# Kernel tuning notes

Hardware: AMD Instinct MI355X
Metric: run time of the kernel (lower is better)

The kernel has to match this reference:

```python
import jax, jax.numpy as jnp
import numpy as np

M, NQ, NK = 2, 1024, 1024
DX, DT = 256, 2
H, D = 8, 32          # num_heads, head_dim
KH = 32               # kernel MLP hidden width
SCALE = D ** -0.5


def setup_inputs() -> dict:
    key = jax.random.key(0)
    ks = jax.random.split(key, 16)
    p = 0.02
    return {
        "xq": jax.random.normal(ks[0], (M, NQ, DX), jnp.float32),
        "xk": jax.random.normal(ks[1], (M, NK, DX), jnp.float32),
        "xv": jax.random.normal(ks[2], (M, NK, DX), jnp.float32),
        "tq": jax.random.normal(ks[3], (M, NQ, DT), jnp.float32),
        "tk": jax.random.normal(ks[4], (M, NK, DT), jnp.float32),
        # projections (no bias, as in nn.Linear(..., bias=False))
        "Wq": jax.random.normal(ks[5], (DX, H * D), jnp.float32) * p,
        "Wk": jax.random.normal(ks[6], (DX, H * D), jnp.float32) * p,
        "Wv": jax.random.normal(ks[7], (DX, H * D), jnp.float32) * p,
        # output projection (with bias)
        "Wo": jax.random.normal(ks[8], (H * D, DX), jnp.float32) * p,
        "bo": jnp.zeros((DX,), jnp.float32),
        # kernel MLP: dt -> KH -> H
        "Wk1": jax.random.normal(ks[9], (DT, KH), jnp.float32) * 0.5,
        "bk1": jnp.zeros((KH,), jnp.float32),
        "Wk2": jax.random.normal(ks[10], (KH, H), jnp.float32) * 0.5,
        "bk2": jnp.zeros((H,), jnp.float32),
        # phi_t: H -> DT
        "Wphi": jax.random.normal(ks[11], (H, DT), jnp.float32) * p,
        "bphi": jnp.zeros((DT,), jnp.float32),
    }


def reference(xq, xk, xv, tq, tk, Wq, Wk, Wv, Wo, bo, Wk1, bk1, Wk2, bk2, Wphi, bphi):
    m, nq, _ = xq.shape
    nk = xk.shape[1]
    # translation group action: diff [m, nq, nk, dt]
    diff = tq[:, :, None, :] - tk[:, None, :, :]
    # q, k: [m, h, n, d]
    q = (xq @ Wq).reshape(m, nq, H, D).transpose(0, 2, 1, 3)
    k = (xk @ Wk).reshape(m, nk, H, D).transpose(0, 2, 1, 3)
    token_dots = jnp.einsum("bhqd,bhkd->bhqk", q, k) * SCALE
    # kernel MLP bias evaluated densely over diffs -> [m, nq, nk, h] -> [m, h, nq, nk]
    hdn = jax.nn.relu(diff @ Wk1 + bk1)
    kdots = (hdn @ Wk2 + bk2).transpose(0, 3, 1, 2)
    dots = kdots + token_dots
    attn = jax.nn.softmax(dots, axis=-1)  # [m, h, nq, nk]
    v = (xv @ Wv).reshape(m, nk, H, D).transpose(0, 2, 1, 3)
    out = jnp.einsum("bhqk,bhkd->bhqd", attn, v)
    out = out.transpose(0, 2, 1, 3).reshape(m, nq, H * D)
    out = out @ Wo + bo  # dropout p=0
    # phi_t path: attn -> [m, nq, nk, h] -> per-pair dt weights
    attn_t = attn.transpose(0, 2, 3, 1)
    t_dots = attn_t @ Wphi + bphi  # [m, nq, nk, dt]
    tq_new = tq + (1.0 / nk) * jnp.sum(diff * t_dots, axis=-2)
    return out, tq_new
```

## Files before the change

kernel.cpp:

```cpp
#include <hip/hip_runtime.h>
#include <hip/hip_bf16.h>

#define MB 2
#define NQ 1024
#define NK 1024
#define DXC 256
#define HD 256
#define HH 8
#define DD 32
#define KHC 32
#define LOG2E 1.4426950408889634f
#define QSCALE 0.25503472301046627f

#define QB 32
#define KB 32
#define KSPLIT 8
#define KL 128
#define NCHUNK 4

#define QPB_F   0u
#define KPB_F   262144u
#define VPT_F   524288u
#define WT_F    786432u
#define AQH_F   917504u
#define BKH_F   950272u
#define TS_F    983040u
#define TKX_F   983048u
#define W2T_F   986120u
#define PART_F  986376u

typedef float f32x4 __attribute__((ext_vector_type(4)));
typedef short bf16x8 __attribute__((ext_vector_type(8)));
typedef _Float16 f16x8 __attribute__((ext_vector_type(8)));
typedef _Float16 f16x2 __attribute__((ext_vector_type(2)));

#define MFMA(a, b, c)   __builtin_amdgcn_mfma_f32_16x16x32_bf16(a, b, c, 0, 0, 0)
#define MFMA16(a, b, c) __builtin_amdgcn_mfma_f32_16x16x32_f16(a, b, c, 0, 0, 0)
#define EXP2(x) exp2f(x)

#define KDQ 36
#define KDH 1160

struct Ptrs {
    const float *xq, *xk, *xv, *tq, *tk;
    const float *Wq, *Wk, *Wv, *Wo, *bo;
    const float *Wk1, *bk1, *Wk2, *bk2, *Wphi, *bphi;
    float* wsf;
    float* out;
};

__device__ __forceinline__ uint cvt_pk_bf16(float lo, float hi) {
    uint r;
    asm("v_cvt_pk_bf16_f32 %0, %1, %2" : "=v"(r) : "v"(lo), "v"(hi));
    return r;
}
__device__ __forceinline__ ushort f2bf1(float f) { return (ushort)cvt_pk_bf16(f, 0.f); }
__device__ __forceinline__ float bf2f(uint x) {
    return __uint_as_float((x & 0xffffu) << 16);
}
__device__ __forceinline__ ushort f2h(float f) {
    _Float16 h = (_Float16)f;
    return __builtin_bit_cast(ushort, h);
}

__global__ __launch_bounds__(256, 4) void k_phase1(Ptrs p) {
    __shared__ __align__(16) float sW[64][65];
    const int u = blockIdx.x;
    const int t = threadIdx.x;
    ushort* wt  = (ushort*)(p.wsf + WT_F);
    ushort* aqh = (ushort*)(p.wsf + AQH_F);
    ushort* bkh = (ushort*)(p.wsf + BKH_F);
    ushort* tkx = (ushort*)(p.wsf + TKX_F);
    ushort* w2t = (ushort*)(p.wsf + W2T_F);
    float*  ts  = p.wsf + TS_F;

    if (u < 64) {
        const int mat = u >> 4;
        const float* W = (mat == 0) ? p.Wq : (mat == 1) ? p.Wk : (mat == 2) ? p.Wv : p.Wo;
        const int k0 = (u & 3) * 64, c0 = ((u >> 2) & 3) * 64;
        #pragma unroll
        for (int i = 0; i < 4; ++i) {
            int flat = i * 1024 + t * 4;
            int r = flat >> 6, c = flat & 63;
            float4 v4 = *(const float4*)(W + (size_t)(k0 + r) * 256 + c0 + c);
            sW[r][c] = v4.x; sW[r][c + 1] = v4.y; sW[r][c + 2] = v4.z; sW[r][c + 3] = v4.w;
        }
        __syncthreads();
        #pragma unroll
        for (int i = 0; i < 4; ++i) {
            int flat = i * 1024 + t * 4;
            int cc = flat >> 6, kk = flat & 63;
            uint2 pk;
            pk.x = cvt_pk_bf16(sW[kk][cc], sW[kk + 1][cc]);
            pk.y = cvt_pk_bf16(sW[kk + 2][cc], sW[kk + 3][cc]);
            *(uint2*)(wt + (size_t)mat * 65536 + (size_t)(c0 + cc) * 256 + k0 + kk) = pk;
        }
    } else if (u < 320) {
        int gid = (u - 64) * 256 + t;
        int row = gid >> 5, j = gid & 31;
        aqh[gid] = f2h(p.tq[row * 2] * p.Wk1[j] + p.tq[row * 2 + 1] * p.Wk1[KHC + j] + p.bk1[j]);
        bkh[gid] = f2h(p.tk[row * 2] * p.Wk1[j] + p.tk[row * 2 + 1] * p.Wk1[KHC + j]);
    } else if (u < 344) {
        int g = (u - 320) * 256 + t;
        int mm = g / 3072, rr = (g % 3072) >> 10, kk = g & 1023;
        float v = (rr == 0) ? p.tk[(size_t)(mm * NK + kk) * 2]
                : (rr == 1) ? p.tk[(size_t)(mm * NK + kk) * 2 + 1] : 1.0f;
        tkx[g] = f2bf1(v);
    } else if (u == 344) {
        for (int g = t; g < 512; g += 256) {
            int hh2 = g >> 5, jj = g & 31;
            w2t[g] = f2h(hh2 < HH ? p.Wk2[jj * HH + hh2] * LOG2E : 0.f);
        }
    } else {
        const int m = u - 345;
        const int c = t & 1, kk = t >> 1;
        float s = 0.f;
        #pragma unroll
        for (int i = 0; i < 8; ++i) s += p.tk[(size_t)(m * NK + kk + i * 128) * 2 + c];
        float* red = (float*)&sW[0][0];
        red[t] = s; __syncthreads();
        for (int off = 128; off >= 2; off >>= 1) {
            if (t < off) red[t] += red[t + off];
            __syncthreads();
        }
        if (t < 2) ts[m * 2 + t] = red[t];
    }
}

__global__ __launch_bounds__(256, 4) void k_phase2(Ptrs p) {
    __shared__ __align__(16) ushort sTr[256][24];
    const int u = blockIdx.x;
    const int t = threadIdx.x;
    ushort* qpb = (ushort*)(p.wsf + QPB_F);
    ushort* kpb = (ushort*)(p.wsf + KPB_F);
    ushort* vpt = (ushort*)(p.wsf + VPT_F);
    const ushort* wt = (const ushort*)(p.wsf + WT_F);

    const int z = u / 128;
    const int R0 = (u % 128) * 16;
    const float* x = (z == 0) ? p.xq : (z == 1) ? p.xk : p.xv;
    const ushort* wz = wt + (size_t)z * 65536;
    const int wid = t >> 6, l = t & 63, g = l >> 4, c16 = l & 15;
    const int wc = wid * 64;
    const int row = R0 + c16;

    f32x4 acc[4];
    #pragma unroll
    for (int i = 0; i < 4; ++i) acc[i] = (f32x4){0.f, 0.f, 0.f, 0.f};

    for (int k0 = 0; k0 < DXC; k0 += 32) {
        const float* xr = x + (size_t)row * DXC + k0 + g * 8;
        float4 a0 = *(const float4*)xr;
        float4 a1 = *(const float4*)(xr + 4);
        union { bf16x8 v; uint d[4]; } af;
        af.d[0] = cvt_pk_bf16(a0.x, a0.y);
        af.d[1] = cvt_pk_bf16(a0.z, a0.w);
        af.d[2] = cvt_pk_bf16(a1.x, a1.y);
        af.d[3] = cvt_pk_bf16(a1.z, a1.w);
        #pragma unroll
        for (int cf = 0; cf < 4; ++cf) {
            bf16x8 bf = *(const bf16x8*)(wz + (size_t)(wc + cf * 16 + c16) * 256 + k0 + g * 8);
            acc[cf] = MFMA(af.v, bf, acc[cf]);
        }
    }
    if (z != 2) {
        #pragma unroll
        for (int cf = 0; cf < 4; ++cf) {
            #pragma unroll
            for (int r = 0; r < 4; ++r) {
                int orow = R0 + g * 4 + r;
                int col = wc + cf * 16 + c16;
                float v = acc[cf][r];
                if (z == 0) qpb[(size_t)orow * HD + col] = f2bf1(v * QSCALE);
                else        kpb[(size_t)orow * HD + col] = f2bf1(v);
            }
        }
    } else {
        #pragma unroll
        for (int cf = 0; cf < 4; ++cf)
            #pragma unroll
            for (int r = 0; r < 4; ++r)
                sTr[wc + cf * 16 + c16][g * 4 + r] = f2bf1(acc[cf][r]);
        __syncthreads();
        const int mq = R0 >> 10, rin = R0 & 1023;
        ushort* dst = vpt + (size_t)mq * (HD * NK) + (size_t)t * NK + rin;
        *(uint4*)dst       = *(const uint4*)&sTr[t][0];
        *(uint4*)(dst + 8) = *(const uint4*)&sTr[t][8];
    }
}

__global__ __launch_bounds__(256, 2) void k_phase3(Ptrs p) {
    __shared__ __align__(16) char smem[47360];
    const int u = blockIdx.x;
    const int t = threadIdx.x;

    const ushort* qpb = (const ushort*)(p.wsf + QPB_F);
    const ushort* kpb = (const ushort*)(p.wsf + KPB_F);
    const ushort* vpt = (const ushort*)(p.wsf + VPT_F);
    const ushort* aqh = (const ushort*)(p.wsf + AQH_F);
    const ushort* bkh = (const ushort*)(p.wsf + BKH_F);
    const ushort* tkx = (const ushort*)(p.wsf + TKX_F);
    const ushort* w2t = (const ushort*)(p.wsf + W2T_F);
    ushort* part = (ushort*)(p.wsf + PART_F);

    const int ks = u & 7;
    const int qt = (u >> 3) & 31;
    const int m  = u >> 8;
    const int q0 = qt * QB;
    const int kbase = ks * KL;
    const int wid = t >> 6;
    const int l = t & 63;
    const int g = l >> 4;
    const int c16 = l & 15;

    ushort* KD0 = (ushort*)smem;
    ushort* KD1 = (ushort*)(smem + 18560);
    ushort (*sP)[32][40] = (ushort(*)[32][40])(smem + 37120);

    f16x8 w2v = *(const f16x8*)(w2t + c16 * 32 + g * 8);
    const float b2l = (c16 < HH) ? p.bk2[c16] * LOG2E : 0.f;
    const f16x8 zero8 = {0, 0, 0, 0, 0, 0, 0, 0};

    bf16x8 qb[2][2];
    #pragma unroll
    for (int hh = 0; hh < 2; ++hh)
        #pragma unroll
        for (int qf = 0; qf < 2; ++qf)
            qb[hh][qf] = *(const bf16x8*)(qpb + (size_t)(m * NQ + q0 + qf * 16 + c16) * HD
                                              + (wid * 2 + hh) * DD + g * 8);
    f16x8 aqv[8];
    #pragma unroll
    for (int qi = 0; qi < 8; ++qi)
        aqv[qi] = *(const f16x8*)(aqh + (size_t)(m * NQ + q0 + wid * 8 + qi) * KHC + g * 8);

    struct BkOps { f16x8 b0, b1; };
    struct KavOps { bf16x8 ka0[2], ka1[2], v0[2], v1[2], vt; };
    const size_t vbase = (size_t)m * (HD * NK);
    const size_t tbase = (size_t)m * 3072 + (size_t)(c16 < 2 ? c16 : 2) * NK;

    auto loadBk = [&](int k0) {
        BkOps c;
        c.b0 = *(const f16x8*)(bkh + (size_t)(m * NK + k0 + c16) * KHC + g * 8);
        c.b1 = *(const f16x8*)(bkh + (size_t)(m * NK + k0 + 16 + c16) * KHC + g * 8);
        return c;
    };
    auto loadKav = [&](int k0) {
        KavOps c;
        #pragma unroll
        for (int hh = 0; hh < 2; ++hh) {
            const int h = wid * 2 + hh;
            c.ka0[hh] = *(const bf16x8*)(kpb + (size_t)(m * NK + k0 + c16) * HD + h * DD + g * 8);
            c.ka1[hh] = *(const bf16x8*)(kpb + (size_t)(m * NK + k0 + 16 + c16) * HD + h * DD + g * 8);
            c.v0[hh]  = *(const bf16x8*)(vpt + vbase + (size_t)(h * DD + c16) * NK + k0 + g * 8);
            c.v1[hh]  = *(const bf16x8*)(vpt + vbase + (size_t)(h * DD + 16 + c16) * NK + k0 + g * 8);
        }
        c.vt = *(const bf16x8*)(tkx + tbase + k0 + g * 8);
        return c;
    };

    f32x4 oacc[2][2][3];
    #pragma unroll
    for (int a = 0; a < 2; ++a)
        #pragma unroll
        for (int bb = 0; bb < 2; ++bb)
            #pragma unroll
            for (int c = 0; c < 3; ++c)
                oacc[a][bb][c] = (f32x4){0.f, 0.f, 0.f, 0.f};

    auto kdPhase = [&](const BkOps& bk, ushort* kdb) {
        __builtin_amdgcn_s_setprio(1);
        #pragma unroll
        for (int qi = 0; qi < 8; ++qi) {
            const int q = wid * 8 + qi;
            #pragma unroll
            for (int kh = 0; kh < 2; ++kh) {
                f16x8 d = aqv[qi] - (kh ? bk.b1 : bk.b0);
                f16x8 hv = __builtin_elementwise_max(d, zero8);
                f32x4 c = {b2l, b2l, b2l, b2l};
                c = MFMA16(hv, w2v, c);
                if (c16 < HH) {
                    uint2 st;
                    st.x = __builtin_bit_cast(uint, __builtin_amdgcn_cvt_pkrtz(c[0], c[1]));
                    st.y = __builtin_bit_cast(uint, __builtin_amdgcn_cvt_pkrtz(c[2], c[3]));
                    *(uint2*)&kdb[c16 * KDH + q * KDQ + kh * 16 + g * 4] = st;
                }
            }
        }
        __builtin_amdgcn_s_setprio(0);
    };
    auto qkpv = [&](const KavOps& kv, const ushort* kdbuf) {
        __builtin_amdgcn_s_setprio(1);
        #pragma unroll
        for (int hh = 0; hh < 2; ++hh) {
            const int h = wid * 2 + hh;
            const ushort* kdb = &kdbuf[h * KDH];
            #pragma unroll
            for (int kf = 0; kf < 2; ++kf) {
                #pragma unroll
                for (int qf = 0; qf < 2; ++qf) {
                    uint2 kd2 = *(const uint2*)&kdb[(qf * 16 + c16) * KDQ + kf * 16 + g * 4];
                    f16x2 k01 = __builtin_bit_cast(f16x2, kd2.x);
                    f16x2 k23 = __builtin_bit_cast(f16x2, kd2.y);
                    f32x4 cinit = {(float)k01[0], (float)k01[1], (float)k23[0], (float)k23[1]};
                    f32x4 s = MFMA((kf ? kv.ka1[hh] : kv.ka0[hh]), qb[hh][qf], cinit);
                    uint2 pk;
                    pk.x = cvt_pk_bf16(EXP2(s[0]), EXP2(s[1]));
                    pk.y = cvt_pk_bf16(EXP2(s[2]), EXP2(s[3]));
                    *(uint2*)&sP[wid][qf * 16 + c16][kf * 16 + g * 4] = pk;
                }
            }
            #pragma unroll
            for (int qf = 0; qf < 2; ++qf) {
                bf16x8 pa = *(const bf16x8*)&sP[wid][qf * 16 + c16][g * 8];
                oacc[hh][qf][0] = MFMA(pa, kv.v0[hh], oacc[hh][qf][0]);
                oacc[hh][qf][1] = MFMA(pa, kv.v1[hh], oacc[hh][qf][1]);
                oacc[hh][qf][2] = MFMA(pa, kv.vt, oacc[hh][qf][2]);
            }
        }
        __builtin_amdgcn_s_setprio(0);
    };

    BkOps bk0v = loadBk(kbase);
    KavOps kv0 = loadKav(kbase);
    BkOps bk1v = loadBk(kbase + KB);
    KavOps kv1 = loadKav(kbase + KB);
    kdPhase(bk0v, KD0);
    __syncthreads();

    kdPhase(bk1v, KD1);
    BkOps bk2v = loadBk(kbase + 2 * KB);
    qkpv(kv0, KD0);
    kv0 = loadKav(kbase + 2 * KB);
    __syncthreads();
    kdPhase(bk2v, KD0);
    BkOps bk3v = loadBk(kbase + 3 * KB);
    qkpv(kv1, KD1);
    kv1 = loadKav(kbase + 3 * KB);
    __syncthreads();
    kdPhase(bk3v, KD1);
    qkpv(kv0, KD0);
    __syncthreads();
    qkpv(kv1, KD1);

    #pragma unroll
    for (int hh = 0; hh < 2; ++hh) {
        int mh = m * HH + wid * 2 + hh;
        #pragma unroll
        for (int qf = 0; qf < 2; ++qf) {
            #pragma unroll
            for (int r = 0; r < 4; ++r) {
                int q = q0 + qf * 16 + g * 4 + r;
                ushort* pb = part + ((size_t)(mh * KSPLIT + ks) * NQ + q) * 40;
                pb[c16]      = f2bf1(oacc[hh][qf][0][r]);
                pb[16 + c16] = f2bf1(oacc[hh][qf][1][r]);
                float e = oacc[hh][qf][2][r];
                if (c16 < 2) pb[32 + c16] = f2bf1(e);
                else if (c16 == 2) *(float*)(pb + 34) = e;
            }
        }
    }
}

__global__ __launch_bounds__(256, 4) void k_phase4(Ptrs p) {
    __shared__ __align__(16) ushort sHob[16][264];
    __shared__ float sD[8][8][2];
    const int u = blockIdx.x;
    const int t = threadIdx.x;
    const ushort* part = (const ushort*)(p.wsf + PART_F);
    const ushort* wt = (const ushort*)(p.wsf + WT_F);
    const float* ts = p.wsf + TS_F;
    float* tq_out = p.out + (size_t)MB * NQ * HD;

    const int m = u >> 7;
    const int q0 = (u & 127) * 8;

    if (t < 128) {
        const int h = t >> 4, dgrp = (t >> 3) & 1, qloc = t & 7;
        const int q = q0 + qloc;
        const int mh = m * HH + h;
        float accO[16] = {};
        float aT = 0.f, lsum = 0.f;
        for (int s = 0; s < KSPLIT; ++s) {
            const ushort* ps = part + ((size_t)(mh * KSPLIT + s) * NQ + q) * 40;
            uint4 v0 = *(const uint4*)(ps + dgrp * 16);
            uint4 v1 = *(const uint4*)(ps + dgrp * 16 + 8);
            accO[0] += bf2f(v0.x); accO[1] += bf2f(v0.x >> 16);
            accO[2] += bf2f(v0.y); accO[3] += bf2f(v0.y >> 16);
            accO[4] += bf2f(v0.z); accO[5] += bf2f(v0.z >> 16);
            accO[6] += bf2f(v0.w); accO[7] += bf2f(v0.w >> 16);
            accO[8] += bf2f(v1.x); accO[9] += bf2f(v1.x >> 16);
            accO[10] += bf2f(v1.y); accO[11] += bf2f(v1.y >> 16);
            accO[12] += bf2f(v1.z); accO[13] += bf2f(v1.z >> 16);
            accO[14] += bf2f(v1.w); accO[15] += bf2f(v1.w >> 16);
            uint at = *(const uint*)(ps + 32);
            aT += bf2f(dgrp == 0 ? at : (at >> 16));
            lsum += *(const float*)(ps + 34);
        }
        const float inv = 1.f / lsum;
        uint dd[8];
        #pragma unroll
        for (int i = 0; i < 8; ++i)
            dd[i] = cvt_pk_bf16(accO[2 * i] * inv, accO[2 * i + 1] * inv);
        ushort* hp = &sHob[qloc][h * DD + dgrp * 16];
        *(uint4*)hp       = (uint4){dd[0], dd[1], dd[2], dd[3]};
        *(uint4*)(hp + 8) = (uint4){dd[4], dd[5], dd[6], dd[7]};
        const float A = aT * inv;
        const float tqc = p.tq[(size_t)(m * NQ + q) * 2 + dgrp];
        sD[h][qloc][dgrp] = p.Wphi[h * 2 + dgrp] * (tqc - A);
    } else {
        for (int i = t - 128; i < 8 * 264; i += 128)
            (&sHob[8][0])[i] = 0;
    }
    __syncthreads();

    if (t < 16) {
        int ql2 = t >> 1, c = t & 1;
        float s = 0.f;
        #pragma unroll
        for (int hh2 = 0; hh2 < 8; ++hh2) s += sD[hh2][ql2][c];
        int qg = q0 + ql2;
        float tqv = p.tq[(size_t)(m * NQ + qg) * 2 + c];
        const float invnk = 1.f / (float)NK;
        tq_out[(size_t)(m * NQ + qg) * 2 + c] =
            tqv + s * invnk + p.bphi[c] * (tqv - ts[m * 2 + c] * invnk);
    }

    const ushort* wz3 = wt + (size_t)3 * 65536;
    const int wid = t >> 6, l = t & 63, g = l >> 4, c16 = l & 15;
    f32x4 acc[4];
    #pragma unroll
    for (int i = 0; i < 4; ++i) acc[i] = (f32x4){0.f, 0.f, 0.f, 0.f};
    for (int k0 = 0; k0 < HD; k0 += 32) {
        bf16x8 af = *(const bf16x8*)&sHob[c16][k0 + g * 8];
        #pragma unroll
        for (int cf = 0; cf < 4; ++cf) {
            int col = wid * 64 + cf * 16 + c16;
            bf16x8 bf = *(const bf16x8*)(wz3 + (size_t)col * 256 + k0 + g * 8);
            acc[cf] = MFMA(af, bf, acc[cf]);
        }
    }
    if (g < 2) {
        #pragma unroll
        for (int cf = 0; cf < 4; ++cf) {
            int col = wid * 64 + cf * 16 + c16;
            float bv = p.bo[col];
            #pragma unroll
            for (int r = 0; r < 4; ++r) {
                int orow = q0 + g * 4 + r;
                p.out[(size_t)(m * NQ + orow) * DXC + col] = acc[cf][r] + bv;
            }
        }
    }
}

extern "C" void kernel_launch(void* const* d_in, const int* in_sizes, int n_in,
                              void* d_out, int out_size, void* d_ws, size_t ws_size,
                              hipStream_t stream)
{
    Ptrs p;
    p.xq   = (const float*)d_in[0];
    p.xk   = (const float*)d_in[1];
    p.xv   = (const float*)d_in[2];
    p.tq   = (const float*)d_in[3];
    p.tk   = (const float*)d_in[4];
    p.Wq   = (const float*)d_in[5];
    p.Wk   = (const float*)d_in[6];
    p.Wv   = (const float*)d_in[7];
    p.Wo   = (const float*)d_in[8];
    p.bo   = (const float*)d_in[9];
    p.Wk1  = (const float*)d_in[10];
    p.bk1  = (const float*)d_in[11];
    p.Wk2  = (const float*)d_in[12];
    p.bk2  = (const float*)d_in[13];
    p.Wphi = (const float*)d_in[14];
    p.bphi = (const float*)d_in[15];
    p.wsf  = (float*)d_ws;
    p.out  = (float*)d_out;

    hipLaunchKernelGGL(k_phase1, dim3(347), dim3(256), 0, stream, p);
    hipLaunchKernelGGL(k_phase2, dim3(384), dim3(256), 0, stream, p);
    hipLaunchKernelGGL(k_phase3, dim3(512), dim3(256), 0, stream, p);
    hipLaunchKernelGGL(k_phase4, dim3(256), dim3(256), 0, stream, p);
}
```

Before: 56.55 us.

## Split phase3 attention across eight waves with one head per wave

The attention phase kernel grows from 256 to 512 threads per block. Each wave now handles one head instead of two, and the kernel-MLP bias computation is split over 8 waves with 4 queries each. This halves per-thread register state (q fragments, K/V operands, accumulators) and doubles the waves available to hide memory and MFMA latency. In exchange, shared memory per block grows for the extra per-wave P tiles, and the tighter launch bound may cap registers or limit resident blocks.

```diff
diff --git a/kernel.cpp b/kernel.cpp
--- a/kernel.cpp
+++ b/kernel.cpp
@@ -189,8 +189,8 @@
     }
 }
 
-__global__ __launch_bounds__(256, 2) void k_phase3(Ptrs p) {
-    __shared__ __align__(16) char smem[47360];
+__global__ __launch_bounds__(512, 4) void k_phase3(Ptrs p) {
+    __shared__ __align__(16) char smem[57600];
     const int u = blockIdx.x;
     const int t = threadIdx.x;
 
@@ -212,6 +212,7 @@
     const int l = t & 63;
     const int g = l >> 4;
     const int c16 = l & 15;
+    const int h = wid;
 
     ushort* KD0 = (ushort*)smem;
     ushort* KD1 = (ushort*)(smem + 18560);
@@ -221,20 +222,18 @@
     const float b2l = (c16 < HH) ? p.bk2[c16] * LOG2E : 0.f;
     const f16x8 zero8 = {0, 0, 0, 0, 0, 0, 0, 0};
 
-    bf16x8 qb[2][2];
+    bf16x8 qb[2];
     #pragma unroll
-    for (int hh = 0; hh < 2; ++hh)
-        #pragma unroll
-        for (int qf = 0; qf < 2; ++qf)
-            qb[hh][qf] = *(const bf16x8*)(qpb + (size_t)(m * NQ + q0 + qf * 16 + c16) * HD
-                                              + (wid * 2 + hh) * DD + g * 8);
-    f16x8 aqv[8];
+    for (int qf = 0; qf < 2; ++qf)
+        qb[qf] = *(const bf16x8*)(qpb + (size_t)(m * NQ + q0 + qf * 16 + c16) * HD
+                                      + h * DD + g * 8);
+    f16x8 aqv[4];
     #pragma unroll
-    for (int qi = 0; qi < 8; ++qi)
-        aqv[qi] = *(const f16x8*)(aqh + (size_t)(m * NQ + q0 + wid * 8 + qi) * KHC + g * 8);
+    for (int qi = 0; qi < 4; ++qi)
+        aqv[qi] = *(const f16x8*)(aqh + (size_t)(m * NQ + q0 + wid * 4 + qi) * KHC + g * 8);
 
     struct BkOps { f16x8 b0, b1; };
-    struct KavOps { bf16x8 ka0[2], ka1[2], v0[2], v1[2], vt; };
+    struct KavOps { bf16x8 ka0, ka1, v0, v1, vt; };
     const size_t vbase = (size_t)m * (HD * NK);
     const size_t tbase = (size_t)m * 3072 + (size_t)(c16 < 2 ? c16 : 2) * NK;
 
@@ -246,32 +245,26 @@
     };
     auto loadKav = [&](int k0) {
         KavOps c;
-        #pragma unroll
-        for (int hh = 0; hh < 2; ++hh) {
-            const int h = wid * 2 + hh;
-            c.ka0[hh] = *(const bf16x8*)(kpb + (size_t)(m * NK + k0 + c16) * HD + h * DD + g * 8);
-            c.ka1[hh] = *(const bf16x8*)(kpb + (size_t)(m * NK + k0 + 16 + c16) * HD + h * DD + g * 8);
-            c.v0[hh]  = *(const bf16x8*)(vpt + vbase + (size_t)(h * DD + c16) * NK + k0 + g * 8);
-            c.v1[hh]  = *(const bf16x8*)(vpt + vbase + (size_t)(h * DD + 16 + c16) * NK + k0 + g * 8);
-        }
-        c.vt = *(const bf16x8*)(tkx + tbase + k0 + g * 8);
+        c.ka0 = *(const bf16x8*)(kpb + (size_t)(m * NK + k0 + c16) * HD + h * DD + g * 8);
+        c.ka1 = *(const bf16x8*)(kpb + (size_t)(m * NK + k0 + 16 + c16) * HD + h * DD + g * 8);
+        c.v0  = *(const bf16x8*)(vpt + vbase + (size_t)(h * DD + c16) * NK + k0 + g * 8);
+        c.v1  = *(const bf16x8*)(vpt + vbase + (size_t)(h * DD + 16 + c16) * NK + k0 + g * 8);
+        c.vt  = *(const bf16x8*)(tkx + tbase + k0 + g * 8);
         return c;
     };
 
-    f32x4 oacc[2][2][3];
+    f32x4 oacc[2][3];
     #pragma unroll
-    for (int a = 0; a < 2; ++a)
-        #pragma unroll
-        for (int bb = 0; bb < 2; ++bb)
-            #pragma unroll
-            for (int c = 0; c < 3; ++c)
-                oacc[a][bb][c] = (f32x4){0.f, 0.f, 0.f, 0.f};
+    for (int bb = 0; bb < 2; ++bb)
+        #pragma unroll
+        for (int c = 0; c < 3; ++c)
+            oacc[bb][c] = (f32x4){0.f, 0.f, 0.f, 0.f};
 
     auto kdPhase = [&](const BkOps& bk, ushort* kdb) {
         __builtin_amdgcn_s_setprio(1);
         #pragma unroll
-        for (int qi = 0; qi < 8; ++qi) {
-            const int q = wid * 8 + qi;
+        for (int qi = 0; qi < 4; ++qi) {
+            const int q = wid * 4 + qi;
             #pragma unroll
             for (int kh = 0; kh < 2; ++kh) {
                 f16x8 d = aqv[qi] - (kh ? bk.b1 : bk.b0);
@@ -290,32 +283,28 @@
     };
     auto qkpv = [&](const KavOps& kv, const ushort* kdbuf) {
         __builtin_amdgcn_s_setprio(1);
-        #pragma unroll
-        for (int hh = 0; hh < 2; ++hh) {
-            const int h = wid * 2 + hh;
-            const ushort* kdb = &kdbuf[h * KDH];
-            #pragma unroll
-            for (int kf = 0; kf < 2; ++kf) {
-                #pragma unroll
-                for (int qf = 0; qf < 2; ++qf) {
-                    uint2 kd2 = *(const uint2*)&kdb[(qf * 16 + c16) * KDQ + kf * 16 + g * 4];
-                    f16x2 k01 = __builtin_bit_cast(f16x2, kd2.x);
-                    f16x2 k23 = __builtin_bit_cast(f16x2, kd2.y);
-                    f32x4 cinit = {(float)k01[0], (float)k01[1], (float)k23[0], (float)k23[1]};
-                    f32x4 s = MFMA((kf ? kv.ka1[hh] : kv.ka0[hh]), qb[hh][qf], cinit);
-                    uint2 pk;
-                    pk.x = cvt_pk_bf16(EXP2(s[0]), EXP2(s[1]));
-                    pk.y = cvt_pk_bf16(EXP2(s[2]), EXP2(s[3]));
-                    *(uint2*)&sP[wid][qf * 16 + c16][kf * 16 + g * 4] = pk;
-                }
+        const ushort* kdb = &kdbuf[h * KDH];
+        #pragma unroll
+        for (int kf = 0; kf < 2; ++kf) {
+            #pragma unroll
+            for (int qf = 0; qf < 2; ++qf) {
+                uint2 kd2 = *(const uint2*)&kdb[(qf * 16 + c16) * KDQ + kf * 16 + g * 4];
+                f16x2 k01 = __builtin_bit_cast(f16x2, kd2.x);
+                f16x2 k23 = __builtin_bit_cast(f16x2, kd2.y);
+                f32x4 cinit = {(float)k01[0], (float)k01[1], (float)k23[0], (float)k23[1]};
+                f32x4 s = MFMA((kf ? kv.ka1 : kv.ka0), qb[qf], cinit);
+                uint2 pk;
+                pk.x = cvt_pk_bf16(EXP2(s[0]), EXP2(s[1]));
+                pk.y = cvt_pk_bf16(EXP2(s[2]), EXP2(s[3]));
+                *(uint2*)&sP[wid][qf * 16 + c16][kf * 16 + g * 4] = pk;
             }
-            #pragma unroll
-            for (int qf = 0; qf < 2; ++qf) {
-                bf16x8 pa = *(const bf16x8*)&sP[wid][qf * 16 + c16][g * 8];
-                oacc[hh][qf][0] = MFMA(pa, kv.v0[hh], oacc[hh][qf][0]);
-                oacc[hh][qf][1] = MFMA(pa, kv.v1[hh], oacc[hh][qf][1]);
-                oacc[hh][qf][2] = MFMA(pa, kv.vt, oacc[hh][qf][2]);
-            }
+        }
+        #pragma unroll
+        for (int qf = 0; qf < 2; ++qf) {
+            bf16x8 pa = *(const bf16x8*)&sP[wid][qf * 16 + c16][g * 8];
+            oacc[qf][0] = MFMA(pa, kv.v0, oacc[qf][0]);
+            oacc[qf][1] = MFMA(pa, kv.v1, oacc[qf][1]);
+            oacc[qf][2] = MFMA(pa, kv.vt, oacc[qf][2]);
         }
         __builtin_amdgcn_s_setprio(0);
     };
@@ -342,18 +331,17 @@
     __syncthreads();
     qkpv(kv1, KD1);
 
-    #pragma unroll
-    for (int hh = 0; hh < 2; ++hh) {
-        int mh = m * HH + wid * 2 + hh;
+    {
+        const int mh = m * HH + h;
         #pragma unroll
         for (int qf = 0; qf < 2; ++qf) {
             #pragma unroll
             for (int r = 0; r < 4; ++r) {
                 int q = q0 + qf * 16 + g * 4 + r;
                 ushort* pb = part + ((size_t)(mh * KSPLIT + ks) * NQ + q) * 40;
-                pb[c16]      = f2bf1(oacc[hh][qf][0][r]);
-                pb[16 + c16] = f2bf1(oacc[hh][qf][1][r]);
-                float e = oacc[hh][qf][2][r];
+                pb[c16]      = f2bf1(oacc[qf][0][r]);
+                pb[16 + c16] = f2bf1(oacc[qf][1][r]);
+                float e = oacc[qf][2][r];
                 if (c16 < 2) pb[32 + c16] = f2bf1(e);
                 else if (c16 == 2) *(float*)(pb + 34) = e;
             }
@@ -479,6 +467,6 @@
 
     hipLaunchKernelGGL(k_phase1, dim3(347), dim3(256), 0, stream, p);
     hipLaunchKernelGGL(k_phase2, dim3(384), dim3(256), 0, stream, p);
-    hipLaunchKernelGGL(k_phase3, dim3(512), dim3(256), 0, stream, p);
+    hipLaunchKernelGGL(k_phase3, dim3(512), dim3(512), 0, stream, p);
     hipLaunchKernelGGL(k_phase4, dim3(256), dim3(256), 0, stream, p);
 }
```

Result: faster. 55.27 us (-2.3%).
